# Performance work log

Measured on AMD Instinct MI355X. Metric: run time of the kernel, lower is better.

Reference implementation:

```python
import jax, jax.numpy as jnp
import numpy as np
from jax import lax

SUR_BETA = 4.0
THRESH = 1.0
ALPHA = float(np.exp(-1.0 / 20.0))  # membrane decay, tau_mem=20
BETA = float(np.exp(-1.0 / 5.0))    # synaptic decay, tau_syn=5

@jax.custom_vjp
def spike(x):
    return (x >= 0).astype(jnp.float32)

def _spike_fwd(x):
    return spike(x), x

def _spike_bwd(x, g):
    e = jnp.exp(-SUR_BETA * jnp.abs(x))
    sg = SUR_BETA * e / (2.0 * (1.0 + e) ** 2)
    return (g * sg,)

spike.defvjp(_spike_fwd, _spike_bwd)

def lif_layer(x, W, b):
    # x: [B, T, Din] -> spikes [B, T, H]
    xt = jnp.einsum('bti,ih->bth', x, W) + b
    B, T, H = xt.shape
    z = jnp.zeros((B, H), xt.dtype)
    def step(carry, x_t):
        v, i = carry
        i = BETA * i + x_t
        v = ALPHA * v + i
        s = spike(v - THRESH)
        v = v * (1.0 - s)  # multiplicative reset
        return (v, i), s
    _, sp = lax.scan(step, (z, z), xt.transpose(1, 0, 2))
    return sp.transpose(1, 0, 2)

def layer_norm(x, scale, bias, eps=1e-6):
    m = jnp.mean(x, axis=-1, keepdims=True)
    v = jnp.mean((x - m) ** 2, axis=-1, keepdims=True)
    return (x - m) / jnp.sqrt(v + eps) * scale + bias

def setup_inputs() -> dict:
    key = jax.random.key(0)
    ks = jax.random.split(key, 6)
    B, T, S, F = 64, 512, 64, 16
    D = S * F  # 1024
    def w(k, shape, fan):
        return (jax.random.normal(k, shape, jnp.float32) / np.sqrt(fan)).astype(jnp.float32)
    return dict(
        spike_trains=(jax.random.uniform(ks[0], (B, T, S, F)) < 0.2).astype(jnp.float32),
        W0=w(ks[1], (D, 256), D), b0=jnp.zeros((256,), jnp.float32),
        W1=w(ks[2], (256, 128), 256), b1=jnp.zeros((128,), jnp.float32),
        W2=w(ks[3], (128, 64), 128), b2=jnp.zeros((64,), jnp.float32),
        ln1_scale=jnp.ones((256,), jnp.float32), ln1_bias=jnp.zeros((256,), jnp.float32),
        ln2_scale=jnp.ones((128,), jnp.float32), ln2_bias=jnp.zeros((128,), jnp.float32),
        Wc=w(ks[4], (B, 2), B), bc=jnp.zeros((2,), jnp.float32),
    )

def reference(spike_trains, W0, b0, W1, b1, W2, b2,
              ln1_scale, ln1_bias, ln2_scale, ln2_bias, Wc, bc):
    B, T, S, F = spike_trains.shape
    x = spike_trains.reshape(B, T, S * F)
    x = lif_layer(x, W0, b0)                                   # [B,T,256]
    x = lif_layer(layer_norm(x, ln1_scale, ln1_bias), W1, b1)  # [B,T,128]
    x = lif_layer(layer_norm(x, ln2_scale, ln2_bias), W2, b2)  # [B,T,64]
    pooled = jnp.mean(x, axis=(1, 2))  # [B]  (faithful to source: mean over time AND hidden)
    logits = pooled @ Wc + bc          # [num_classes] -- classifier sees batch as feature dim
    return (logits, pooled, jnp.mean(x))
```

## Files before the change

kernel.cpp:

```cpp
#include <hip/hip_runtime.h>

#define T_STEPS 512
#define BATCH 64

__device__ constexpr float ALPHA_ = 0.95122942450071400910f;
__device__ constexpr float BETA_  = 0.81873075307798185867f;

typedef __attribute__((ext_vector_type(8))) short bf16x8;
typedef __attribute__((ext_vector_type(4))) float f32x4;

__device__ inline unsigned short f2bf_rne(float f) {
  union { float f; unsigned int u; } v{f};
  const unsigned int u = v.u;
  return (unsigned short)((u + 0x7FFFu + ((u >> 16) & 1u)) >> 16);
}
__device__ inline float bf2f(unsigned short h) {
  union { unsigned int u; float f; } v{(unsigned int)h << 16};
  return v.f;
}

__device__ inline void gload16(const void* g, void* l) {
  __builtin_amdgcn_global_load_lds(
      (const __attribute__((address_space(1))) unsigned int*)g,
      (__attribute__((address_space(3))) unsigned int*)l, 16, 0, 0);
}

__device__ inline unsigned int pkbf(float first, float second) {
#if __has_builtin(__builtin_amdgcn_perm)
  return __builtin_amdgcn_perm(__float_as_uint(second), __float_as_uint(first),
                               0x07060302u);
#else
  return (__float_as_uint(first) >> 16) | (__float_as_uint(second) & 0xFFFF0000u);
#endif
}

__device__ inline bf16x8 cvt_frag(const f32x4 lo, const f32x4 hi) {
  union { unsigned int w[4]; bf16x8 v; } u;
  u.w[0] = pkbf(lo.x, lo.y);
  u.w[1] = pkbf(lo.z, lo.w);
  u.w[2] = pkbf(hi.x, hi.y);
  u.w[3] = pkbf(hi.z, hi.w);
  return u.v;
}

template <int WM, int WC, int TM, bool A_F32, bool LNFOLD>
__global__ __launch_bounds__(256) void gemm_deep2(
    const void* __restrict__ Av, const char* __restrict__ Bhi,
    const char* __restrict__ Blo, const float* __restrict__ uvec,
    const float* __restrict__ cvec, float* __restrict__ C, int N, int K) {
  constexpr int BM = WM * TM;
  constexpr int FM = TM / 16;
  constexpr int ABY = A_F32 ? BM * 128 : BM * 64;
  constexpr int AIP = ABY / 4096;
  constexpr int ASTEP = A_F32 ? 128 : 64;
  constexpr int W2N = AIP + 16;
  __shared__ char smem[3 * ABY];

  const int tid = threadIdx.x;
  const int lane = tid & 63;
  const int wave = tid >> 6;
  const int wm = wave / WC, wc = wave % WC;
  const int l15 = lane & 15, l4 = lane >> 4;
  const int row0 = blockIdx.y * BM;
  const int col0 = blockIdx.x * (WC * 64);
  const int KB = K / 32;

  const char* Ab = (const char*)Av;

  const char* a_src[AIP];
#pragma unroll
  for (int i = 0; i < AIP; ++i) {
    const int unit = i * 256 + tid;
    if constexpr (A_F32) {
      const int fr = unit >> 7, h = (unit >> 6) & 1, ln = unit & 63;
      a_src[i] = Ab + ((size_t)(row0 + fr * 16 + (ln & 15)) * K + ((ln >> 4) * 8)) * 4 + h * 16;
    } else {
      const int r = ((unit >> 6) << 4) | (unit & 15);
      const int j = (unit >> 4) & 3;
      a_src[i] = Ab + ((size_t)(row0 + r) * K + j * 8) * 2;
    }
  }
  const char* bh_base = Bhi + (size_t)(blockIdx.x * WC + wc) * KB * 4096 + (size_t)lane * 16;
  const char* bl_base = Blo + (size_t)(blockIdx.x * WC + wc) * KB * 4096 + (size_t)lane * 16;

  int aoff = 0, boff = 0;
  const int amax = (KB - 1) * ASTEP;
  const int bmax = (KB - 1) * 4096;

  f32x4 acc[FM][4] = {};
  f32x4 acc1[FM] = {};
  const bf16x8 ONES = {0x3F80, 0x3F80, 0x3F80, 0x3F80,
                       0x3F80, 0x3F80, 0x3F80, 0x3F80};
  bf16x8 bh0[4], bl0[4], bh1[4], bl1[4];

#define SB __builtin_amdgcn_sched_barrier(0)

#define STAGE_A(buf)                                                   \
  do {                                                                 \
    _Pragma("unroll") for (int i = 0; i < AIP; ++i)                    \
        gload16(a_src[i] + aoff, (buf) + (i * 256 + tid) * 16);        \
  } while (0)

#define LOAD_B(bh, bl, off_)                                           \
  do {                                                                 \
    const char* ph = bh_base + (off_);                                 \
    const char* pl = bl_base + (off_);                                 \
    bh[0] = *(const bf16x8*)(ph);                                      \
    bh[1] = *(const bf16x8*)(ph + 1024);                               \
    bh[2] = *(const bf16x8*)(ph + 2048);                               \
    bh[3] = *(const bf16x8*)(ph + 3072);                               \
    bl[0] = *(const bf16x8*)(pl);                                      \
    bl[1] = *(const bf16x8*)(pl + 1024);                               \
    bl[2] = *(const bf16x8*)(pl + 2048);                               \
    bl[3] = *(const bf16x8*)(pl + 3072);                               \
  } while (0)

  char* bufR = smem;
  char* bufM = smem + ABY;
  char* bufS = smem + 2 * ABY;

  SB;
  STAGE_A(bufR);
  SB;
  LOAD_B(bh0, bl0, 0);
  SB;
  aoff = ASTEP;
  STAGE_A(bufM);
  SB;
  LOAD_B(bh1, bl1, 4096);
  SB;
  aoff = (2 * ASTEP < amax) ? 2 * ASTEP : amax;
  boff = (2 * 4096 < bmax) ? 2 * 4096 : bmax;
  asm volatile("s_waitcnt vmcnt(%0)" ::"i"(W2N) : "memory");
  __builtin_amdgcn_s_barrier();
  SB;

#define KSTEP(BH, BL)                                                        \
  do {                                                                       \
    STAGE_A(bufS);                                              \
    aoff = (aoff < amax) ? aoff + ASTEP : aoff;                              \
    SB;                                                                      \
    bf16x8 af[FM];                                                           \
    _Pragma("unroll") for (int m = 0; m < FM; ++m) {                         \
      const int fr = wm * FM + m;                                            \
      if constexpr (A_F32) {                                                 \
        const f32x4 lo = *(const f32x4*)(bufR + ((fr * 2 + 0) * 64 + lane) * 16); \
        const f32x4 hi = *(const f32x4*)(bufR + ((fr * 2 + 1) * 64 + lane) * 16); \
        af[m] = cvt_frag(lo, hi);                                            \
      } else {                                                               \
        af[m] = *(const bf16x8*)(bufR + (fr * 64 + lane) * 16);              \
      }                                                                      \
    }                                                                        \
    SB;                                                                      \
    _Pragma("unroll") for (int m = 0; m < FM; ++m) {                         \
      _Pragma("unroll") for (int n = 0; n < 4; ++n) {                        \
        acc[m][n] = __builtin_amdgcn_mfma_f32_16x16x32_bf16(af[m], BH[n],    \
                                                            acc[m][n], 0, 0, 0); \
        acc[m][n] = __builtin_amdgcn_mfma_f32_16x16x32_bf16(af[m], BL[n],    \
                                                            acc[m][n], 0, 0, 0); \
      }                                                                      \
      if constexpr (LNFOLD)                                                  \
        acc1[m] = __builtin_amdgcn_mfma_f32_16x16x32_bf16(af[m], ONES,       \
                                                          acc1[m], 0, 0, 0); \
    }                                                                        \
    SB;                                                                      \
    LOAD_B(BH, BL, boff);            \
    boff = (boff < bmax) ? boff + 4096 : boff;                               \
    SB;                                                                      \
    asm volatile("s_waitcnt vmcnt(%0)" ::"i"(W2N) : "memory");               \
    __builtin_amdgcn_s_barrier();                                            \
    SB;                                                                      \
    { char* t = bufR; bufR = bufM; bufM = bufS; bufS = t; }                  \
  } while (0)

  const int ITER = KB / 2;
  for (int it = 0; it < ITER; ++it) {
    KSTEP(bh0, bl0);
    KSTEP(bh1, bl1);
  }
  asm volatile("s_waitcnt vmcnt(0) lgkmcnt(0)" ::: "memory");

#undef KSTEP
#undef LOAD_B
#undef STAGE_A
#undef SB

  const int row0w = row0 + wm * TM;
  const int col0w = col0 + wc * 64;
#pragma unroll
  for (int m = 0; m < FM; ++m) {
    const int rbase = row0w + m * 16 + l4 * 4;
    float iv[4], mv[4];
    if constexpr (LNFOLD) {
#pragma unroll
      for (int r = 0; r < 4; ++r) {
        const float mean = acc1[m][r] / (float)K;
        const float inv = 1.0f / sqrtf(mean * (1.f - mean) + 1e-6f);
        iv[r] = inv;
        mv[r] = mean * inv;
      }
    }
#pragma unroll
    for (int n = 0; n < 4; ++n) {
      const int c = col0w + n * 16 + l15;
      const float cc = cvec[c];
      float uu = 0.f;
      if constexpr (LNFOLD) uu = uvec[c];
#pragma unroll
      for (int r = 0; r < 4; ++r) {
        float v;
        if constexpr (LNFOLD) v = iv[r] * acc[m][n][r] - mv[r] * uu + cc;
        else v = acc[m][n][r] + cc;
        C[(size_t)(rbase + r) * N + c] = v;
      }
    }
  }
}

__global__ void prep_split(const float* __restrict__ W, const float* __restrict__ s,
                           char* __restrict__ hi, char* __restrict__ lo,
                           int K, int N) {
  const int g = blockIdx.x * 256 + threadIdx.x;
  const int total = (K * N) / 8;
  if (g >= total) return;
  constexpr int UB = 256;
  const int KB = K / 32;
  const int unit = g % UB;
  const int kb = (g / UB) % KB;
  const int cb = g / (UB * KB);
  const int n = cb * 64 + ((unit >> 6) << 4) + (unit & 15);
  const int kbase = kb * 32 + ((unit >> 4) & 3) * 8;
  short h8[8], l8[8];
#pragma unroll
  for (int jj = 0; jj < 8; ++jj) {
    const int k = kbase + jj;
    float w = W[(size_t)k * N + n];
    if (s) w *= s[k];
    const unsigned short hb = f2bf_rne(w);
    const unsigned short lb = f2bf_rne(w - bf2f(hb));
    h8[jj] = (short)hb;
    l8[jj] = (short)lb;
  }
  *(bf16x8*)(hi + (size_t)g * 16) = *(const bf16x8*)h8;
  *(bf16x8*)(lo + (size_t)g * 16) = *(const bf16x8*)l8;
}

__global__ __launch_bounds__(256) void prep_consts(
    const float* __restrict__ W, const float* __restrict__ s,
    const float* __restrict__ b, const float* __restrict__ bias2,
    float* __restrict__ u, float* __restrict__ c, int K, int N) {
  const int n = blockIdx.x;
  const int t = threadIdx.x;
  float us = 0.f, cs = 0.f;
  for (int k = t; k < K; k += 256) {
    const float w = W[(size_t)k * N + n];
    us += s[k] * w;
    cs += b[k] * w;
  }
  __shared__ float su[256], sc[256];
  su[t] = us;
  sc[t] = cs;
  __syncthreads();
  for (int o = 128; o > 0; o >>= 1) {
    if (t < o) { su[t] += su[t + o]; sc[t] += sc[t + o]; }
    __syncthreads();
  }
  if (t == 0) { u[n] = su[0]; c[n] = sc[0] + bias2[n]; }
}

template <int H, bool SPIKE_OUT, bool ACCUM>
__global__ void lif_scan(const float* __restrict__ xt,
                         unsigned short* __restrict__ sp,
                         float* __restrict__ tsum) {
  const int n = blockIdx.x * 64 + threadIdx.x;
  const int b = n / H, h = n % H;
  const float* p = xt + (size_t)b * T_STEPS * H + h;
  unsigned short* q = nullptr;
  if constexpr (SPIKE_OUT) q = sp + (size_t)b * T_STEPS * H + h;

  float v = 0.f, cur = 0.f, ts = 0.f;
  for (int t = 0; t < T_STEPS; t += 32) {
    float x[32];
#pragma unroll
    for (int u = 0; u < 32; ++u) x[u] = p[(size_t)u * H];
#pragma unroll
    for (int u = 0; u < 32; ++u) {
      cur = BETA_ * cur + x[u];
      v = ALPHA_ * v + cur;
      const bool sb = (v >= 1.f);
      if constexpr (SPIKE_OUT) q[(size_t)u * H] = sb ? 0x3F80 : 0;
      if constexpr (ACCUM) ts += sb ? 1.f : 0.f;
      v = sb ? 0.f : v;
    }
    p += (size_t)32 * H;
    if constexpr (SPIKE_OUT) q += (size_t)32 * H;
  }
  if constexpr (ACCUM) tsum[n] = ts;
}

__global__ void finalize(const float* __restrict__ tsum,
                         const float* __restrict__ Wc,
                         const float* __restrict__ bc,
                         float* __restrict__ out) {
  const int b = threadIdx.x;
  float s = 0.f;
#pragma unroll 8
  for (int h = 0; h < 64; ++h) s += tsum[b * 64 + h];
  const float pooled = s * (1.0f / (512.f * 64.f));
  out[2 + b] = pooled;

  float tot = pooled;
  float l0 = pooled * Wc[b * 2 + 0];
  float l1 = pooled * Wc[b * 2 + 1];
#pragma unroll
  for (int off = 32; off > 0; off >>= 1) {
    tot += __shfl_xor(tot, off);
    l0 += __shfl_xor(l0, off);
    l1 += __shfl_xor(l1, off);
  }
  if (b == 0) {
    out[0] = l0 + bc[0];
    out[1] = l1 + bc[1];
    out[66] = tot * (1.0f / 64.f);
  }
}

extern "C" void kernel_launch(void* const* d_in, const int* in_sizes, int n_in,
                              void* d_out, int out_size, void* d_ws, size_t ws_size,
                              hipStream_t stream) {
  const float* X    = (const float*)d_in[0];
  const float* W0   = (const float*)d_in[1];
  const float* b0   = (const float*)d_in[2];
  const float* W1   = (const float*)d_in[3];
  const float* b1   = (const float*)d_in[4];
  const float* W2   = (const float*)d_in[5];
  const float* b2   = (const float*)d_in[6];
  const float* ln1s = (const float*)d_in[7];
  const float* ln1b = (const float*)d_in[8];
  const float* ln2s = (const float*)d_in[9];
  const float* ln2b = (const float*)d_in[10];
  const float* Wc   = (const float*)d_in[11];
  const float* bc   = (const float*)d_in[12];
  float* out = (float*)d_out;

  char* w = (char*)d_ws;
  float* buf0 = (float*)w;
  float* buf1 = (float*)w;
  float* buf2 = (float*)(w + 16777216);
  size_t off = 33554432;
  unsigned short* sp0 = (unsigned short*)(w + off); off += 16777216;
  unsigned short* sp1 = (unsigned short*)(w + off); off += 8388608;
  char* hi0 = w + off; off += 524288;
  char* lo0 = w + off; off += 524288;
  char* hi1 = w + off; off += 65536;
  char* lo1 = w + off; off += 65536;
  char* hi2 = w + off; off += 16384;
  char* lo2 = w + off; off += 16384;
  float* u1 = (float*)(w + off); off += 512;
  float* c1 = (float*)(w + off); off += 512;
  float* u2 = (float*)(w + off); off += 256;
  float* c2 = (float*)(w + off); off += 256;
  float* tsum = (float*)(w + off); off += 16384;

  const int M = 32768;

  prep_split<<<128, 256, 0, stream>>>(W0, nullptr, hi0, lo0, 1024, 256);
  prep_split<<<16, 256, 0, stream>>>(W1, ln1s, hi1, lo1, 256, 128);
  prep_split<<<4, 256, 0, stream>>>(W2, ln2s, hi2, lo2, 128, 64);
  prep_consts<<<128, 256, 0, stream>>>(W1, ln1s, ln1b, b1, u1, c1, 256, 128);
  prep_consts<<<64, 256, 0, stream>>>(W2, ln2s, ln2b, b2, u2, c2, 128, 64);

  gemm_deep2<1, 4, 64, true, false><<<dim3(1, M / 64), 256, 0, stream>>>(
      X, hi0, lo0, nullptr, b0, buf0, 256, 1024);
  lif_scan<256, true, false><<<(BATCH * 256) / 64, 64, 0, stream>>>(buf0, sp0, nullptr);

  gemm_deep2<2, 2, 32, false, true><<<dim3(1, M / 64), 256, 0, stream>>>(
      sp0, hi1, lo1, u1, c1, buf1, 128, 256);
  lif_scan<128, true, false><<<(BATCH * 128) / 64, 64, 0, stream>>>(buf1, sp1, nullptr);

  gemm_deep2<4, 1, 32, false, true><<<dim3(1, M / 128), 256, 0, stream>>>(
      sp1, hi2, lo2, u2, c2, buf2, 64, 128);
  lif_scan<64, false, true><<<(BATCH * 64) / 64, 64, 0, stream>>>(buf2, nullptr, tsum);

  finalize<<<1, 64, 0, stream>>>(tsum, Wc, bc, out);
}
```

Baseline: 132.1 us.

## Add split-K intra-block GEMM for first layer and retile second GEMM

Adds a new gemm_splitk kernel for the 1024-deep first projection. Each of four waves handles a quarter of K for a 32x64 output tile with its own triple-buffered LDS staging, and the partial sums are reduced through shared memory. The aim is more blocks (4x1024 grid) and shorter per-wave K loops in place of one block covering all 256 columns. The second GEMM is also relaunched with a different wave arrangement and a 2-column grid. The cost is that A rows are now reloaded once per column block, plus extra LDS traffic for the reduction.

New measurement: 210.5 us. 1.59x slower.

```diff
diff --git a/kernel.cpp b/kernel.cpp
--- a/kernel.cpp
+++ b/kernel.cpp
@@ -41,6 +41,141 @@
   u.w[2] = pkbf(hi.x, hi.y);
   u.w[3] = pkbf(hi.z, hi.w);
   return u.v;
+}
+
+#define SB __builtin_amdgcn_sched_barrier(0)
+
+__global__ __launch_bounds__(256) void gemm_splitk(
+    const float* __restrict__ A, const char* __restrict__ Bhi,
+    const char* __restrict__ Blo, const float* __restrict__ cvec,
+    float* __restrict__ C, int N, int K) {
+  __shared__ char smem[49152];
+  const int tid = threadIdx.x;
+  const int lane = tid & 63;
+  const int wave = tid >> 6;
+  const int l15 = lane & 15, l4 = lane >> 4;
+  const int row0 = blockIdx.y * 32;
+  const int col0 = blockIdx.x * 64;
+  const int KBt = K / 32;
+  const int KBw = KBt / 4;
+  char* wbase = smem + wave * 12288;
+
+  const char* Ab = (const char*)A;
+  const char* a_src[4];
+#pragma unroll
+  for (int i = 0; i < 4; ++i) {
+    const int fr = i >> 1, h = i & 1;
+    a_src[i] = Ab + ((size_t)(row0 + fr * 16 + l15) * K + (size_t)wave * (K / 4) + l4 * 8) * 4 + h * 16;
+  }
+  const char* bh_base = Bhi + ((size_t)blockIdx.x * KBt + wave * KBw) * 4096 + (size_t)lane * 16;
+  const char* bl_base = Blo + ((size_t)blockIdx.x * KBt + wave * KBw) * 4096 + (size_t)lane * 16;
+
+  int aoff = 0, boff = 0;
+  const int amax = (KBw - 1) * 128;
+  const int bmax = (KBw - 1) * 4096;
+
+  f32x4 acc[2][4] = {};
+  bf16x8 bh0[4], bl0[4], bh1[4], bl1[4];
+
+#define STAGE_A0(bufp)                                                  \
+  do {                                                                  \
+    _Pragma("unroll") for (int i = 0; i < 4; ++i)                       \
+        gload16(a_src[i] + aoff, (bufp) + i * 1024 + lane * 16);        \
+  } while (0)
+
+#define LOAD_B0(bh, bl, off_)                                           \
+  do {                                                                  \
+    const char* ph = bh_base + (off_);                                  \
+    const char* pl = bl_base + (off_);                                  \
+    bh[0] = *(const bf16x8*)(ph);                                       \
+    bh[1] = *(const bf16x8*)(ph + 1024);                                \
+    bh[2] = *(const bf16x8*)(ph + 2048);                                \
+    bh[3] = *(const bf16x8*)(ph + 3072);                                \
+    bl[0] = *(const bf16x8*)(pl);                                       \
+    bl[1] = *(const bf16x8*)(pl + 1024);                                \
+    bl[2] = *(const bf16x8*)(pl + 2048);                                \
+    bl[3] = *(const bf16x8*)(pl + 3072);                                \
+  } while (0)
+
+  char* bufR = wbase;
+  char* bufM = wbase + 4096;
+  char* bufS = wbase + 8192;
+
+  SB;
+  STAGE_A0(bufR);
+  SB;
+  LOAD_B0(bh0, bl0, 0);
+  SB;
+  aoff = 128;
+  STAGE_A0(bufM);
+  SB;
+  LOAD_B0(bh1, bl1, 4096);
+  SB;
+  aoff = (256 < amax) ? 256 : amax;
+  boff = (8192 < bmax) ? 8192 : bmax;
+  asm volatile("s_waitcnt vmcnt(20)" ::: "memory");
+  SB;
+
+#define KSTEP0(BH, BL)                                                       \
+  do {                                                                       \
+    STAGE_A0(bufS);                                              \
+    aoff = (aoff < amax) ? aoff + 128 : aoff;                                \
+    SB;                                                                      \
+    bf16x8 af[2];                                                            \
+    _Pragma("unroll") for (int m = 0; m < 2; ++m) {                          \
+      const f32x4 lo = *(const f32x4*)(bufR + ((m * 2 + 0) * 64 + lane) * 16); \
+      const f32x4 hi = *(const f32x4*)(bufR + ((m * 2 + 1) * 64 + lane) * 16); \
+      af[m] = cvt_frag(lo, hi);                                              \
+    }                                                                        \
+    SB;                                                                      \
+    _Pragma("unroll") for (int m = 0; m < 2; ++m) {                          \
+      _Pragma("unroll") for (int n = 0; n < 4; ++n) {                        \
+        acc[m][n] = __builtin_amdgcn_mfma_f32_16x16x32_bf16(af[m], BH[n],    \
+                                                            acc[m][n], 0, 0, 0); \
+        acc[m][n] = __builtin_amdgcn_mfma_f32_16x16x32_bf16(af[m], BL[n],    \
+                                                            acc[m][n], 0, 0, 0); \
+      }                                                                      \
+    }                                                                        \
+    SB;                                                                      \
+    LOAD_B0(BH, BL, boff);                                       \
+    boff = (boff < bmax) ? boff + 4096 : boff;                               \
+    SB;                                                                      \
+    asm volatile("s_waitcnt vmcnt(20)" ::: "memory");  \
+    SB;                                                                      \
+    { char* t = bufR; bufR = bufM; bufM = bufS; bufS = t; }                  \
+  } while (0)
+
+  const int ITER = KBw / 2;
+  for (int it = 0; it < ITER; ++it) {
+    KSTEP0(bh0, bl0);
+    KSTEP0(bh1, bl1);
+  }
+  asm volatile("s_waitcnt vmcnt(0) lgkmcnt(0)" ::: "memory");
+
+#undef KSTEP0
+#undef LOAD_B0
+#undef STAGE_A0
+
+#pragma unroll
+  for (int fr = 0; fr < 2; ++fr)
+#pragma unroll
+    for (int n = 0; n < 4; ++n)
+      *(f32x4*)(wbase + ((fr * 4 + n) * 64 + lane) * 16) = acc[fr][n];
+  __syncthreads();
+
+#pragma unroll
+  for (int fr = 0; fr < 2; ++fr) {
+    f32x4 s = *(const f32x4*)(smem + ((fr * 4 + wave) * 64 + lane) * 16);
+#pragma unroll
+    for (int v = 1; v < 4; ++v)
+      s += *(const f32x4*)(smem + v * 12288 + ((fr * 4 + wave) * 64 + lane) * 16);
+    const int c = col0 + wave * 16 + l15;
+    const float cc = cvec[c];
+    const int rbase = row0 + fr * 16 + l4 * 4;
+#pragma unroll
+    for (int r = 0; r < 4; ++r)
+      C[(size_t)(rbase + r) * N + c] = s[r] + cc;
+  }
 }
 
 template <int WM, int WC, int TM, bool A_F32, bool LNFOLD>
@@ -92,8 +227,6 @@
   const bf16x8 ONES = {0x3F80, 0x3F80, 0x3F80, 0x3F80,
                        0x3F80, 0x3F80, 0x3F80, 0x3F80};
   bf16x8 bh0[4], bl0[4], bh1[4], bl1[4];
-
-#define SB __builtin_amdgcn_sched_barrier(0)
 
 #define STAGE_A(buf)                                                   \
   do {                                                                 \
@@ -164,7 +297,7 @@
                                                           acc1[m], 0, 0, 0); \
     }                                                                        \
     SB;                                                                      \
-    LOAD_B(BH, BL, boff);            \
+    LOAD_B(BH, BL, boff);                                       \
     boff = (boff < bmax) ? boff + 4096 : boff;                               \
     SB;                                                                      \
     asm volatile("s_waitcnt vmcnt(%0)" ::"i"(W2N) : "memory");               \
@@ -183,7 +316,6 @@
 #undef KSTEP
 #undef LOAD_B
 #undef STAGE_A
-#undef SB
 
   const int row0w = row0 + wm * TM;
   const int col0w = col0 + wc * 64;
@@ -370,11 +502,11 @@
   prep_consts<<<128, 256, 0, stream>>>(W1, ln1s, ln1b, b1, u1, c1, 256, 128);
   prep_consts<<<64, 256, 0, stream>>>(W2, ln2s, ln2b, b2, u2, c2, 128, 64);
 
-  gemm_deep2<1, 4, 64, true, false><<<dim3(1, M / 64), 256, 0, stream>>>(
-      X, hi0, lo0, nullptr, b0, buf0, 256, 1024);
+  gemm_splitk<<<dim3(256 / 64, M / 32), 256, 0, stream>>>(
+      X, hi0, lo0, b0, buf0, 256, 1024);
   lif_scan<256, true, false><<<(BATCH * 256) / 64, 64, 0, stream>>>(buf0, sp0, nullptr);
 
-  gemm_deep2<2, 2, 32, false, true><<<dim3(1, M / 64), 256, 0, stream>>>(
+  gemm_deep2<4, 1, 32, false, true><<<dim3(2, M / 128), 256, 0, stream>>>(
       sp0, hi1, lo1, u1, c1, buf1, 128, 256);
   lif_scan<128, true, false><<<(BATCH * 128) / 64, 64, 0, stream>>>(buf1, sp1, nullptr);
 
```

## Add simple LDS-staged GEMM for first layer and retile second GEMM

Applied to the files above, without the earlier changes.

Adds gemm_m97, a single-buffered kernel for the layer-0 projection. Each block covers a 64x128 output tile, stages both A (fp32) and the split-bf16 B through LDS using global_load_lds, and takes 64 K per sync. It replaces the deep-pipelined gemm_deep2 launch, which covered 64x256 per block with B in registers. The layer-1 GEMM is also retiled from 2x2 waves over 64 rows to 4x1 waves over 128 rows with two column blocks. The aim is more parallel blocks and LDS reuse of B, at the cost of losing the triple-buffer overlap and adding barrier stalls.

Result: slower. 159.0 us (+20.3%).

```diff
diff --git a/kernel.cpp b/kernel.cpp
--- a/kernel.cpp
+++ b/kernel.cpp
@@ -42,6 +42,93 @@
   u.w[3] = pkbf(hi.z, hi.w);
   return u.v;
 }
+
+__global__ __launch_bounds__(256) void gemm_m97(
+    const float* __restrict__ A, const char* __restrict__ Bhi,
+    const char* __restrict__ Blo, const float* __restrict__ bias,
+    float* __restrict__ C, int N, int K) {
+  __shared__ char As[16384];
+  __shared__ char Bh[16384];
+  __shared__ char Bl[16384];
+
+  const int tid = threadIdx.x;
+  const int lane = tid & 63;
+  const int wave = tid >> 6;
+  const int wm = wave >> 1, wc = wave & 1;
+  const int l15 = lane & 15, l4 = lane >> 4;
+  const int row0 = blockIdx.y * 64;
+  const int col0 = blockIdx.x * 128;
+  const int KB32 = K / 32;
+  const int KB64 = K / 64;
+
+  const char* Ab = (const char*)A;
+  const char* a_src[2];
+#pragma unroll
+  for (int i = 0; i < 2; ++i) {
+    const int unit = i * 256 + tid;
+    const int fr = unit >> 7, h = (unit >> 6) & 1, ln = unit & 63;
+    a_src[i] = Ab + ((size_t)(row0 + fr * 16 + (ln & 15)) * K + ((ln >> 4) * 8)) * 4 + h * 16;
+  }
+
+  f32x4 acc[2][4] = {};
+
+  for (int kb = 0; kb < KB64; ++kb) {
+    __syncthreads();
+#pragma unroll
+    for (int sub = 0; sub < 2; ++sub) {
+      const int kb32 = kb * 2 + sub;
+#pragma unroll
+      for (int i = 0; i < 2; ++i)
+        gload16(a_src[i] + (size_t)kb32 * 128, As + sub * 8192 + (i * 256 + tid) * 16);
+#pragma unroll
+      for (int g = 0; g < 2; ++g) {
+        const size_t so = ((size_t)(blockIdx.x * 2 + g) * KB32 + kb32) * 4096 + (size_t)tid * 16;
+        gload16(Bhi + so, Bh + (g * 2 + sub) * 4096 + tid * 16);
+        gload16(Blo + so, Bl + (g * 2 + sub) * 4096 + tid * 16);
+      }
+    }
+    __syncthreads();
+
+#pragma unroll
+    for (int ks = 0; ks < 2; ++ks) {
+      bf16x8 af[2], bh[4], bl[4];
+#pragma unroll
+      for (int m = 0; m < 2; ++m) {
+        const int fr = wm * 2 + m;
+        const f32x4 lo = *(const f32x4*)(As + ks * 8192 + ((fr * 2 + 0) * 64 + lane) * 16);
+        const f32x4 hi = *(const f32x4*)(As + ks * 8192 + ((fr * 2 + 1) * 64 + lane) * 16);
+        af[m] = cvt_frag(lo, hi);
+      }
+#pragma unroll
+      for (int n = 0; n < 4; ++n) {
+        bh[n] = *(const bf16x8*)(Bh + (wc * 2 + ks) * 4096 + (n * 64 + lane) * 16);
+        bl[n] = *(const bf16x8*)(Bl + (wc * 2 + ks) * 4096 + (n * 64 + lane) * 16);
+      }
+#pragma unroll
+      for (int m = 0; m < 2; ++m)
+#pragma unroll
+        for (int n = 0; n < 4; ++n) {
+          acc[m][n] = __builtin_amdgcn_mfma_f32_16x16x32_bf16(af[m], bh[n], acc[m][n], 0, 0, 0);
+          acc[m][n] = __builtin_amdgcn_mfma_f32_16x16x32_bf16(af[m], bl[n], acc[m][n], 0, 0, 0);
+        }
+    }
+  }
+
+#pragma unroll
+  for (int m = 0; m < 2; ++m) {
+    const int rbase = row0 + wm * 32 + m * 16 + l4 * 4;
+#pragma unroll
+    for (int n = 0; n < 4; ++n) {
+      const int c = col0 + wc * 64 + n * 16 + l15;
+      const float cc = bias[c];
+#pragma unroll
+      for (int r = 0; r < 4; ++r)
+        C[(size_t)(rbase + r) * N + c] = acc[m][n][r] + cc;
+    }
+  }
+}
+
+#define SB __builtin_amdgcn_sched_barrier(0)
 
 template <int WM, int WC, int TM, bool A_F32, bool LNFOLD>
 __global__ __launch_bounds__(256) void gemm_deep2(
@@ -92,8 +179,6 @@
   const bf16x8 ONES = {0x3F80, 0x3F80, 0x3F80, 0x3F80,
                        0x3F80, 0x3F80, 0x3F80, 0x3F80};
   bf16x8 bh0[4], bl0[4], bh1[4], bl1[4];
-
-#define SB __builtin_amdgcn_sched_barrier(0)
 
 #define STAGE_A(buf)                                                   \
   do {                                                                 \
@@ -164,7 +249,7 @@
                                                           acc1[m], 0, 0, 0); \
     }                                                                        \
     SB;                                                                      \
-    LOAD_B(BH, BL, boff);            \
+    LOAD_B(BH, BL, boff);                                       \
     boff = (boff < bmax) ? boff + 4096 : boff;                               \
     SB;                                                                      \
     asm volatile("s_waitcnt vmcnt(%0)" ::"i"(W2N) : "memory");               \
@@ -183,7 +268,6 @@
 #undef KSTEP
 #undef LOAD_B
 #undef STAGE_A
-#undef SB
 
   const int row0w = row0 + wm * TM;
   const int col0w = col0 + wc * 64;
@@ -370,11 +454,11 @@
   prep_consts<<<128, 256, 0, stream>>>(W1, ln1s, ln1b, b1, u1, c1, 256, 128);
   prep_consts<<<64, 256, 0, stream>>>(W2, ln2s, ln2b, b2, u2, c2, 128, 64);
 
-  gemm_deep2<1, 4, 64, true, false><<<dim3(1, M / 64), 256, 0, stream>>>(
-      X, hi0, lo0, nullptr, b0, buf0, 256, 1024);
+  gemm_m97<<<dim3(2, M / 64), 256, 0, stream>>>(
+      X, hi0, lo0, b0, buf0, 256, 1024);
   lif_scan<256, true, false><<<(BATCH * 256) / 64, 64, 0, stream>>>(buf0, sp0, nullptr);
 
-  gemm_deep2<2, 2, 32, false, true><<<dim3(1, M / 64), 256, 0, stream>>>(
+  gemm_deep2<4, 1, 32, false, true><<<dim3(2, M / 128), 256, 0, stream>>>(
       sp0, hi1, lo1, u1, c1, buf1, 128, 256);
   lif_scan<128, true, false><<<(BATCH * 128) / 64, 64, 0, stream>>>(buf1, sp1, nullptr);
 
```
